# Optimization experiments

Measured on AMD Instinct MI355X. Metric: run time of the kernel, lower is better.

The kernel has to match this reference:

```python
import jax, jax.numpy as jnp
import numpy as np

OUT, IN = 4096, 4096      # weight_shape
VDIM = 8                  # codebook vector_dim
CODEBOOK_SIZE = 256
LEVEL = 2                 # haar_decomposition_level
INV_SQRT2 = 0.7071067811865476


def unpack_bool(packed, shape):
    # packed: int array of bytes (values 0..255); unpack 8 bits per byte (LSB first)
    bits = (packed[:, None] >> jnp.arange(8, dtype=packed.dtype)) & 1  # [n_bytes, 8]
    return bits.reshape(shape)


def inverse_haar(c, level):
    # c: [..., n] orthonormal Haar coefficients laid out [a_L, d_L, d_{L-1}, ..., d_1]
    n = c.shape[-1]
    m = n >> level
    a = c[..., :m]
    while m < n:
        d = c[..., m:2 * m]
        even = (a + d) * INV_SQRT2
        odd = (a - d) * INV_SQRT2
        a = jnp.stack([even, odd], axis=-1).reshape(c.shape[:-1] + (2 * m,))
        m *= 2
    return a


def setup_inputs() -> dict:
    key = jax.random.key(0)
    k1, k2, k3, k4, k5 = jax.random.split(key, 5)
    x = jax.random.normal(k1, (4, 2048, IN), dtype=jnp.float32)
    codebook = jax.random.normal(k2, (CODEBOOK_SIZE, VDIM), dtype=jnp.float32)
    scales = jax.random.uniform(k5, (OUT, 1), dtype=jnp.float32)
    indices = jax.random.randint(k3, (OUT * IN // VDIM,), 0, CODEBOOK_SIZE, dtype=jnp.int32)
    signs_packed = jax.random.randint(k4, (OUT * IN // 8,), 0, 256, dtype=jnp.int32)
    return {"x": x, "codebook": codebook, "scales": scales,
            "indices": indices, "signs_packed": signs_packed}


def reference(x, codebook, scales, indices, signs_packed):
    # codebook gather -> haar-domain magnitudes, reshaped to signs_shape = weight shape
    haar_freq = codebook[indices].reshape(OUT, IN)
    # unpack sign bits and map {0,1} -> {-1,+1}
    signs = 2.0 * unpack_bool(signs_packed, (OUT, IN)).astype(haar_freq.dtype) - 1.0
    haar_freq = haar_freq * signs
    # multi-level inverse Haar wavelet along in_features
    w = inverse_haar(haar_freq, LEVEL)
    w = w * scales  # per-output-row scales
    return jnp.einsum('bsi,oi->bso', x, w)
```

## Files before the change

### kernel.cpp

```cpp
#include <hip/hip_runtime.h>
#include <hip/hip_bf16.h>

typedef unsigned short u16;
typedef unsigned int u32;
typedef float f32x4 __attribute__((ext_vector_type(4)));
typedef u16 u16x4 __attribute__((ext_vector_type(4)));
typedef u16 u16x8 __attribute__((ext_vector_type(8)));
typedef __bf16 bf16x8 __attribute__((ext_vector_type(8)));

#define OUT_DIM 4096
#define IN_DIM  4096
#define M_DIM   8192

__device__ __forceinline__ u16 f2bf(float f) {
  u32 u = __builtin_bit_cast(u32, f);
  return (u16)((u + 0x7FFFu + ((u >> 16) & 1u)) >> 16);
}

__global__ __launch_bounds__(256) void build_w_kernel(
    const float* __restrict__ codebook, const float* __restrict__ scales,
    const int* __restrict__ indices, const int* __restrict__ signs,
    u16* __restrict__ W) {
  __shared__ float c[IN_DIM];
  const int o   = blockIdx.x;
  const int tid = threadIdx.x;
  for (int g = tid; g < IN_DIM / 8; g += 256) {
    const int idx = indices[o * (IN_DIM / 8) + g];
    const int sp  = signs[o * (IN_DIM / 8) + g];
    f32x4 c0 = *(const f32x4*)&codebook[idx * 8];
    f32x4 c1 = *(const f32x4*)&codebook[idx * 8 + 4];
    float v[8] = {c0[0], c0[1], c0[2], c0[3], c1[0], c1[1], c1[2], c1[3]};
#pragma unroll
    for (int j = 0; j < 8; ++j)
      c[g * 8 + j] = ((sp >> j) & 1) ? v[j] : -v[j];
  }
  __syncthreads();
  const float scale = scales[o];
  const float S = 0.70710678118654752440f;
  for (int t = tid; t < IN_DIM / 4; t += 256) {
    float a   = c[t];
    float d1  = c[IN_DIM / 4 + t];
    float d2a = c[IN_DIM / 2 + 2 * t];
    float d2b = c[IN_DIM / 2 + 2 * t + 1];
    float e  = (a + d1) * S;
    float od = (a - d1) * S;
    u16x4 w;
    w[0] = f2bf((e  + d2a) * S * scale);
    w[1] = f2bf((e  - d2a) * S * scale);
    w[2] = f2bf((od + d2b) * S * scale);
    w[3] = f2bf((od - d2b) * S * scale);
    *(u16x4*)&W[(size_t)o * IN_DIM + 4 * t] = w;
  }
}

__global__ __launch_bounds__(256) void cvt_x_kernel(
    const float* __restrict__ X, u16* __restrict__ Xb) {
  const int stride = gridDim.x * blockDim.x;
  const int n8 = (M_DIM * IN_DIM) / 8;
  for (int i = blockIdx.x * blockDim.x + threadIdx.x; i < n8; i += stride) {
    f32x4 a = *(const f32x4*)&X[(size_t)i * 8];
    f32x4 b = *(const f32x4*)&X[(size_t)i * 8 + 4];
    u16x8 r;
    r[0] = f2bf(a[0]); r[1] = f2bf(a[1]); r[2] = f2bf(a[2]); r[3] = f2bf(a[3]);
    r[4] = f2bf(b[0]); r[5] = f2bf(b[1]); r[6] = f2bf(b[2]); r[7] = f2bf(b[3]);
    *(u16x8*)&Xb[(size_t)i * 8] = r;
  }
}

__global__ __launch_bounds__(512, 1) void gemm_bt_kernel(
    const u16* __restrict__ A,
    const u16* __restrict__ B,
    float*     __restrict__ C) {
  constexpr int K   = IN_DIM;
  constexpr int NT  = K / 64;
  constexpr int NIT = NT / 2;
  extern __shared__ char smem[];

  const int tid  = threadIdx.x;
  const int wave = tid >> 6;
  const int lane = tid & 63;

  const int swz = (blockIdx.x & 7) * 64 + (blockIdx.x >> 3);
  const int bm = (swz >> 4) * 256;
  const int bn = (swz & 15) * 256;

  const int wr  = (wave >> 2) * 128;
  const int wc  = (wave & 3) * 64;
  const int fr  = lane & 15;
  const int fkB = (lane >> 4) * 16;

  int offA[2][4], offB[4];
#pragma unroll
  for (int mq = 0; mq < 2; ++mq)
#pragma unroll
    for (int m = 0; m < 4; ++m) {
      int o = (wr + mq * 64 + m * 16 + fr) * 64 + fkB;
      offA[mq][m] = o ^ ((o >> 3) & 0x30);
    }
#pragma unroll
  for (int n = 0; n < 4; ++n) {
    int o = (wc + n * 16 + fr) * 64 + fkB;
    offB[n] = 16384 + (o ^ ((o >> 3) & 0x30));
  }

  const int d0 = tid * 16,        d1 = 8192 + tid * 16;
  const int l0 = d0 ^ ((d0 >> 3) & 0x30), l1 = d1 ^ ((d1 >> 3) & 0x30);
  const u16* srcA0 = A + (size_t)(bm + (d0 >> 6)) * K + ((l0 & 63) >> 1);
  const u16* srcA1 = A + (size_t)(bm + (d1 >> 6)) * K + ((l1 & 63) >> 1);
  const u16* srcB0 = B + (size_t)(bn + (d0 >> 6)) * K + ((l0 & 63) >> 1);
  const u16* srcB1 = B + (size_t)(bn + (d1 >> 6)) * K + ((l1 & 63) >> 1);
  const int ldsW = wave * 1024;

#define GLD(SRC, DST)                                              \
  __builtin_amdgcn_global_load_lds(                                \
      (const __attribute__((address_space(1))) void*)(SRC),        \
      (__attribute__((address_space(3))) void*)(DST), 16, 0, 0)

  auto stageRegion = [&](int bufi, int ks, int tile) {
    char* base = smem + bufi * 65536 + ks * 32768 + ldsW;
    const u16* a0 = srcA0 + tile * 64 + ks * 32;
    const u16* a1 = srcA1 + tile * 64 + ks * 32;
    const u16* b0 = srcB0 + tile * 64 + ks * 32;
    const u16* b1 = srcB1 + tile * 64 + ks * 32;
    GLD(a0, base);
    GLD(a1, base + 8192);
    GLD(b0, base + 16384);
    GLD(b1, base + 24576);
  };

  f32x4 acc[8][4] = {};
  bf16x8 aq[4], bq[4];

  stageRegion(0, 0, 0);
  stageRegion(0, 1, 0);
  stageRegion(1, 0, 1);
  asm volatile("s_waitcnt vmcnt(4)" ::: "memory");
  __builtin_amdgcn_s_barrier();

#define PHASE(BUFI, KS, MQ, READB, STAGE, GATE)                              \
  {                                                                          \
    const char* rb = smem + (BUFI) * 65536 + (KS) * 32768;                   \
    if (READB) {                                                             \
      _Pragma("unroll")                                                      \
      for (int n = 0; n < 4; ++n) bq[n] = *(const bf16x8*)(rb + offB[n]);    \
    }                                                                        \
    _Pragma("unroll")                                                        \
    for (int m = 0; m < 4; ++m) aq[m] = *(const bf16x8*)(rb + offA[MQ][m]);  \
    STAGE;                                                                   \
    __builtin_amdgcn_s_barrier();                                            \
    asm volatile("s_waitcnt lgkmcnt(0)" ::: "memory");                       \
    __builtin_amdgcn_s_setprio(1);                                           \
    _Pragma("unroll")                                                        \
    for (int m = 0; m < 4; ++m)                                              \
      _Pragma("unroll")                                                      \
      for (int n = 0; n < 4; ++n)                                            \
        acc[(MQ) * 4 + m][n] = __builtin_amdgcn_mfma_f32_16x16x32_bf16(      \
            aq[m], bq[n], acc[(MQ) * 4 + m][n], 0, 0, 0);                    \
    __builtin_amdgcn_s_setprio(0);                                           \
    GATE;                                                                    \
    __builtin_amdgcn_s_barrier();                                            \
  }

  for (int i = 0; i < NIT - 1; ++i) {
    const int t0 = 2 * i;
    PHASE(0, 0, 0, 1, stageRegion(1, 1, t0 + 1), )
    PHASE(0, 0, 1, 0, , )
    PHASE(0, 1, 0, 1, stageRegion(0, 0, t0 + 2), )
    PHASE(0, 1, 1, 0, ,
          asm volatile("s_waitcnt vmcnt(4)" ::: "memory"); )
    PHASE(1, 0, 0, 1, stageRegion(0, 1, t0 + 2), )
    PHASE(1, 0, 1, 0, , )
    PHASE(1, 1, 0, 1, stageRegion(1, 0, t0 + 3), )
    PHASE(1, 1, 1, 0, ,
          asm volatile("s_waitcnt vmcnt(4)" ::: "memory"); )
  }

  PHASE(0, 0, 0, 1, stageRegion(1, 1, NT - 1), )
  PHASE(0, 0, 1, 0, , )
  PHASE(0, 1, 0, 1, , )
  PHASE(0, 1, 1, 0, ,
        asm volatile("s_waitcnt vmcnt(0)" ::: "memory"); )
  PHASE(1, 0, 0, 1, , )
  PHASE(1, 0, 1, 0, , )
  PHASE(1, 1, 0, 1, , )
  PHASE(1, 1, 1, 0, , )
#undef PHASE
#undef GLD

#pragma unroll
  for (int h = 0; h < 8; ++h)
#pragma unroll
    for (int n = 0; n < 4; ++n) {
      const int col = bn + wc + n * 16 + fr;
#pragma unroll
      for (int j = 0; j < 4; ++j) {
        const int row = bm + wr + h * 16 + (lane >> 4) * 4 + j;
        C[(size_t)row * OUT_DIM + col] = acc[h][n][j];
      }
    }
}

extern "C" void kernel_launch(void* const* d_in, const int* in_sizes, int n_in,
                              void* d_out, int out_size, void* d_ws, size_t ws_size,
                              hipStream_t stream) {
  const float* x        = (const float*)d_in[0];
  const float* codebook = (const float*)d_in[1];
  const float* scales   = (const float*)d_in[2];
  const int*   indices  = (const int*)d_in[3];
  const int*   signs    = (const int*)d_in[4];
  float* out = (float*)d_out;

  u16* W  = (u16*)d_ws;
  u16* Xb = (u16*)d_ws + (size_t)OUT_DIM * IN_DIM;

  (void)hipFuncSetAttribute((const void*)gemm_bt_kernel,
                            hipFuncAttributeMaxDynamicSharedMemorySize, 131072);

  build_w_kernel<<<OUT_DIM, 256, 0, stream>>>(codebook, scales, indices, signs, W);
  cvt_x_kernel<<<2048, 256, 0, stream>>>(x, Xb);
  gemm_bt_kernel<<<(M_DIM / 256) * (OUT_DIM / 256), 512, 131072, stream>>>(Xb, W, out);
}
```

Measured before the change: 291.1 us.

## Double-buffer LDS fragment registers to overlap LDS reads with MFMA

Restructures the GEMM main loop so that A/B fragments for the next phase are read from LDS into a second register set while MFMAs run on the current set. Partial lgkmcnt waits and sched_barriers replace the full lgkmcnt(0) wait before each MFMA block, and there is now one barrier per phase instead of two. This aims to hide LDS read latency behind matrix math. In exchange it uses more VGPRs and needs careful wait counts to stay correct alongside the global-to-LDS staging.

```diff
diff --git a/kernel.cpp b/kernel.cpp
--- a/kernel.cpp
+++ b/kernel.cpp
@@ -129,62 +129,74 @@
   };
 
   f32x4 acc[8][4] = {};
-  bf16x8 aq[4], bq[4];
+  bf16x8 aq0[4], aq1[4], bq0[4], bq1[4];
+
+#define RD_A(DST, BUFI, KS, MQ)                                              \
+  _Pragma("unroll")                                                          \
+  for (int m = 0; m < 4; ++m)                                                \
+    DST[m] = *(const bf16x8*)(smem + (BUFI) * 65536 + (KS) * 32768 +         \
+                              offA[MQ][m]);
+#define RD_B(DST, BUFI, KS)                                                  \
+  _Pragma("unroll")                                                          \
+  for (int n = 0; n < 4; ++n)                                                \
+    DST[n] = *(const bf16x8*)(smem + (BUFI) * 65536 + (KS) * 32768 +         \
+                              offB[n]);
+#define MM(CA, CB, MQ)                                                       \
+  __builtin_amdgcn_s_setprio(1);                                             \
+  _Pragma("unroll")                                                          \
+  for (int m = 0; m < 4; ++m)                                                \
+    _Pragma("unroll")                                                        \
+    for (int n = 0; n < 4; ++n)                                              \
+      acc[(MQ) * 4 + m][n] = __builtin_amdgcn_mfma_f32_16x16x32_bf16(        \
+          CA[m], CB[n], acc[(MQ) * 4 + m][n], 0, 0, 0);                      \
+  __builtin_amdgcn_s_setprio(0);
+#define BAR                                                                  \
+  __builtin_amdgcn_sched_barrier(0);                                         \
+  __builtin_amdgcn_s_barrier();
+#define LG(N) asm volatile("s_waitcnt lgkmcnt(" #N ")" ::: "memory")
+#define VM(N) asm volatile("s_waitcnt vmcnt(" #N ")" ::: "memory")
 
   stageRegion(0, 0, 0);
   stageRegion(0, 1, 0);
   stageRegion(1, 0, 1);
-  asm volatile("s_waitcnt vmcnt(4)" ::: "memory");
+  VM(4);
   __builtin_amdgcn_s_barrier();
-
-#define PHASE(BUFI, KS, MQ, READB, STAGE, GATE)                              \
-  {                                                                          \
-    const char* rb = smem + (BUFI) * 65536 + (KS) * 32768;                   \
-    if (READB) {                                                             \
-      _Pragma("unroll")                                                      \
-      for (int n = 0; n < 4; ++n) bq[n] = *(const bf16x8*)(rb + offB[n]);    \
-    }                                                                        \
-    _Pragma("unroll")                                                        \
-    for (int m = 0; m < 4; ++m) aq[m] = *(const bf16x8*)(rb + offA[MQ][m]);  \
-    STAGE;                                                                   \
-    __builtin_amdgcn_s_barrier();                                            \
-    asm volatile("s_waitcnt lgkmcnt(0)" ::: "memory");                       \
-    __builtin_amdgcn_s_setprio(1);                                           \
-    _Pragma("unroll")                                                        \
-    for (int m = 0; m < 4; ++m)                                              \
-      _Pragma("unroll")                                                      \
-      for (int n = 0; n < 4; ++n)                                            \
-        acc[(MQ) * 4 + m][n] = __builtin_amdgcn_mfma_f32_16x16x32_bf16(      \
-            aq[m], bq[n], acc[(MQ) * 4 + m][n], 0, 0, 0);                    \
-    __builtin_amdgcn_s_setprio(0);                                           \
-    GATE;                                                                    \
-    __builtin_amdgcn_s_barrier();                                            \
-  }
+  RD_B(bq0, 0, 0)
+  RD_A(aq0, 0, 0, 0)
 
   for (int i = 0; i < NIT - 1; ++i) {
     const int t0 = 2 * i;
-    PHASE(0, 0, 0, 1, stageRegion(1, 1, t0 + 1), )
-    PHASE(0, 0, 1, 0, , )
-    PHASE(0, 1, 0, 1, stageRegion(0, 0, t0 + 2), )
-    PHASE(0, 1, 1, 0, ,
-          asm volatile("s_waitcnt vmcnt(4)" ::: "memory"); )
-    PHASE(1, 0, 0, 1, stageRegion(0, 1, t0 + 2), )
-    PHASE(1, 0, 1, 0, , )
-    PHASE(1, 1, 0, 1, stageRegion(1, 0, t0 + 3), )
-    PHASE(1, 1, 1, 0, ,
-          asm volatile("s_waitcnt vmcnt(4)" ::: "memory"); )
-  }
-
-  PHASE(0, 0, 0, 1, stageRegion(1, 1, NT - 1), )
-  PHASE(0, 0, 1, 0, , )
-  PHASE(0, 1, 0, 1, , )
-  PHASE(0, 1, 1, 0, ,
-        asm volatile("s_waitcnt vmcnt(0)" ::: "memory"); )
-  PHASE(1, 0, 0, 1, , )
-  PHASE(1, 0, 1, 0, , )
-  PHASE(1, 1, 0, 1, , )
-  PHASE(1, 1, 1, 0, , )
-#undef PHASE
+    RD_A(aq1, 0, 0, 1)                                  BAR LG(4); MM(aq0, bq0, 0)
+    RD_B(bq1, 0, 1) RD_A(aq0, 0, 1, 0)
+    stageRegion(1, 1, t0 + 1); VM(4);                   BAR LG(8); MM(aq1, bq0, 1)
+    RD_A(aq1, 0, 1, 1)                                  BAR LG(4); MM(aq0, bq1, 0)
+    RD_B(bq0, 1, 0) RD_A(aq0, 1, 0, 0)
+    stageRegion(0, 0, t0 + 2); VM(4);                   BAR LG(8); MM(aq1, bq1, 1)
+    RD_A(aq1, 1, 0, 1)                                  BAR LG(4); MM(aq0, bq0, 0)
+    RD_B(bq1, 1, 1) RD_A(aq0, 1, 1, 0)
+    stageRegion(0, 1, t0 + 2); VM(4);                   BAR LG(8); MM(aq1, bq0, 1)
+    RD_A(aq1, 1, 1, 1)                                  BAR LG(4); MM(aq0, bq1, 0)
+    RD_B(bq0, 0, 0) RD_A(aq0, 0, 0, 0)
+    stageRegion(1, 0, t0 + 3); VM(4);                   BAR LG(8); MM(aq1, bq1, 1)
+  }
+
+  {
+    RD_A(aq1, 0, 0, 1)                                  BAR LG(4); MM(aq0, bq0, 0)
+    RD_B(bq1, 0, 1) RD_A(aq0, 0, 1, 0)
+    stageRegion(1, 1, NT - 1); VM(4);                   BAR LG(8); MM(aq1, bq0, 1)
+    RD_A(aq1, 0, 1, 1)                                  BAR LG(4); MM(aq0, bq1, 0)
+    RD_B(bq0, 1, 0) RD_A(aq0, 1, 0, 0) VM(0);           BAR LG(8); MM(aq1, bq1, 1)
+    RD_A(aq1, 1, 0, 1)                                  BAR LG(4); MM(aq0, bq0, 0)
+    RD_B(bq1, 1, 1) RD_A(aq0, 1, 1, 0)                  BAR LG(8); MM(aq1, bq0, 1)
+    RD_A(aq1, 1, 1, 1)                                  BAR LG(4); MM(aq0, bq1, 0)
+                                                        BAR LG(0); MM(aq1, bq1, 1)
+  }
+#undef RD_A
+#undef RD_B
+#undef MM
+#undef BAR
+#undef LG
+#undef VM
 #undef GLD
 
 #pragma unroll
```

After: 292.8 us. About the same (+0.6%).
